# Optimization experiments

Measured on AMD Instinct MI355X. Metric: run time of the kernel, lower is better.

Reference implementation:

```python
import jax, jax.numpy as jnp
import numpy as np

B, T, D, H = 64, 512, 1024, 1024


def setup_inputs() -> dict:
    key = jax.random.key(0)
    ks = jax.random.split(key, 6)
    std = 1.0 / np.sqrt(H)  # torch reset_parameters: uniform(-std, std)
    x = jax.random.normal(ks[0], (B, T, D), dtype=jnp.float32)
    teacher_mask = jax.random.uniform(ks[1], (B, T), dtype=jnp.float32)
    Wx = jax.random.uniform(ks[2], (4 * H, D), minval=-std, maxval=std, dtype=jnp.float32)
    bx = jax.random.uniform(ks[3], (4 * H,), minval=-std, maxval=std, dtype=jnp.float32)
    Wh = jax.random.uniform(ks[4], (4 * H, H), minval=-std, maxval=std, dtype=jnp.float32)
    bh = jax.random.uniform(ks[5], (4 * H,), minval=-std, maxval=std, dtype=jnp.float32)
    return {"x": x, "teacher_mask": teacher_mask, "Wx": Wx, "bx": bx, "Wh": Wh, "bh": bh}


def reference(x, teacher_mask, Wx, bx, Wh, bh):
    b = x.shape[0]
    h0 = jnp.zeros((b, H), dtype=x.dtype)
    c0 = jnp.zeros((b, H), dtype=x.dtype)
    xs = jnp.swapaxes(x, 0, 1)                      # [T, B, D]
    ms = jnp.swapaxes(teacher_mask, 0, 1)[..., None]  # [T, B, 1]

    def step(carry, inp):
        hn, cn = carry
        x_t, m = inp
        # teacher_fn(seq, (hn, cn), x_t) := hn (previous hidden); blend with mask
        new_x = m * hn + (1.0 - m) * x_t
        gates = new_x @ Wx.T + bx + hn @ Wh.T + bh   # [B, 4H]
        i, f, g, o = jnp.split(gates, 4, axis=1)     # torch chunk order: i, f, g, o
        i = jax.nn.sigmoid(i)
        f = jax.nn.sigmoid(f)
        g = jnp.tanh(g)
        o = jax.nn.sigmoid(o)
        cy = cn * f + i * g
        hy = o * jnp.tanh(cy)
        return (hy, cy), hy

    (hn, cn), ys = jax.lax.scan(step, (h0, c0), (xs, ms))
    out = jnp.swapaxes(ys, 0, 1)                     # [B, T, H]
    return out, hn, cn
```

## Files before the change

### kernel.cpp

```cpp
#include <hip/hip_runtime.h>
#include <stdint.h>


#define B_ 64
#define T_ 512
#define D_ 1024
#define H_ 1024
#define NBLK 256
#define UPB 8
#define NROW 32
#define NTHR 512

typedef __attribute__((ext_vector_type(8))) short short8;
typedef __attribute__((ext_vector_type(16))) float f32x16;

#define GBUF_OFF 131072
#define BIAS_OFF 147968
#define SMEM_BYTES 148096

#define WS_ABUF 4096
#define PANEL (64 * 2048)

__device__ __forceinline__ unsigned f2bf(float f) {
  unsigned u = __float_as_uint(f);
  return (u + 0x7FFFu + ((u >> 16) & 1u)) >> 16;
}
__device__ __forceinline__ float sigf(float x) { return 1.0f / (1.0f + __expf(-x)); }
__device__ __forceinline__ float tanhf_(float x) { return 1.0f - 2.0f / (__expf(2.0f * x) + 1.0f); }

__global__ void prep_a0(const float* __restrict__ x, const float* __restrict__ tm,
                        unsigned short* __restrict__ abuf) {
  int i = blockIdx.x * blockDim.x + threadIdx.x;
  if (i >= B_ * D_) return;
  int d = i & (D_ - 1), b = i >> 10;
  float m = tm[b * T_];
  float a = (1.0f - m) * x[(size_t)b * T_ * D_ + d];
  abuf[((d >> 3) * 64 + b) * 8 + (d & 7)] = (unsigned short)f2bf(a);
}

__global__ __launch_bounds__(NTHR, 1)
void lstm_persist(const float* __restrict__ xf,
                  const float* __restrict__ tm,
                  const float* __restrict__ Wx, const float* __restrict__ bxp,
                  const float* __restrict__ Wh, const float* __restrict__ bhp,
                  float* __restrict__ out,
                  unsigned short* __restrict__ abuf,
                  unsigned* __restrict__ flags,
                  unsigned* __restrict__ gen)
{
  extern __shared__ char smem[];
  float* gbuf     = (float*)(smem + GBUF_OFF);
  float* bias_lds = (float*)(smem + BIAS_OFF);

  const int tid = threadIdx.x;
  const int bid = blockIdx.x;
  const int ug  = bid >> 1;
  const int bg  = bid & 1;

  for (int i = 0; i < 64; ++i) {
    const int s  = i * NTHR + tid;
    const int dw = s & 3, n = (s >> 2) & 31, kgs = (s >> 7) & 1;
    const int js = (s >> 8) & 15, kos = s >> 12;
    const int grow = (n >> 3) * H_ + ug * UPB + (n & 7);
    const int k = kos * 256 + js * 16 + kgs * 8 + dw * 2;
    const float* src = (k < D_) ? (Wx + (size_t)grow * D_ + k)
                                : (Wh + (size_t)grow * H_ + (k - D_));
    float2 v = *(const float2*)src;
    *(unsigned*)(smem + (size_t)s * 4) = f2bf(v.x) | (f2bf(v.y) << 16);
  }
  if (tid < NROW) {
    const int grow = (tid >> 3) * H_ + ug * UPB + (tid & 7);
    bias_lds[tid] = bxp[grow] + bhp[grow];
  }

  const int lane = tid & 63;
  const int wid  = tid >> 6;
  const int ko   = wid;
  const int l31  = lane & 31;
  const int kg   = lane >> 5;
  const int b0   = bg * 32;

  const unsigned wbase = (unsigned)(ko * 16384 + kg * 512 + l31 * 16);
#define LDW(J) (*(const short8*)(smem + wbase + (unsigned)((J) * 1024)))
  const size_t aull0 = ((size_t)(ko * 32 + kg) * 64 + (b0 + l31)) * 2;

  const int act = (tid < 256);
  const int cb2 = (tid >> 3) & 31;
  const int cu  = tid & 7;
  const int b   = b0 + cb2;
  const int hu  = ug * UPB + cu;
  float ccell = 0.0f, hv = 0.0f;

  unsigned cur = 0;
  __syncthreads();

  for (int t = 0; t < T_; ++t) {
    const int nxt = (t + 1 < T_) ? (t + 1) : t;
    const unsigned tgt = (unsigned)(t + 1);

    const unsigned long long* ap =
        (const unsigned long long*)(abuf + (size_t)cur * PANEL) + aull0;
    short8 af[16];
#pragma unroll
    for (int j = 0; j < 16; ++j) {
      unsigned long long lo = __hip_atomic_load(ap + (size_t)j * 256,
                                                __ATOMIC_RELAXED, __HIP_MEMORY_SCOPE_AGENT);
      unsigned long long hi = __hip_atomic_load(ap + (size_t)j * 256 + 1,
                                                __ATOMIC_RELAXED, __HIP_MEMORY_SCOPE_AGENT);
      ((unsigned long long*)&af[j])[0] = lo;
      ((unsigned long long*)&af[j])[1] = hi;
    }

    f32x16 acc = {0,0,0,0,0,0,0,0,0,0,0,0,0,0,0,0};
#pragma unroll
    for (int j = 0; j < 16; ++j)
      acc = __builtin_amdgcn_mfma_f32_32x32x16_bf16(af[j], LDW(j), acc, 0, 0, 0);

    float mv = 0.0f, xv = 0.0f;
    if (act) {
      mv = tm[b * T_ + nxt];
      xv = xf[((size_t)b * T_ + nxt) * D_ + hu];
    }

    const int s = wid & 3;
    if (wid < 4) {
#pragma unroll
      for (int e = 0; e < 16; ++e) {
        const int br = (e & 3) + 8 * (e >> 2) + 4 * kg;
        float g = acc[e];
        if (wid == 0) g += bias_lds[l31];
        gbuf[(s * 32 + br) * 33 + l31] = g;
      }
    }
    __syncthreads();
    if (wid >= 4) {
#pragma unroll
      for (int e = 0; e < 16; ++e) {
        const int br = (e & 3) + 8 * (e >> 2) + 4 * kg;
        gbuf[(s * 32 + br) * 33 + l31] += acc[e];
      }
    }
    __syncthreads();

    if (act) {
      float gi = 0.0f, gf = 0.0f, gg = 0.0f, go = 0.0f;
#pragma unroll
      for (int sl = 0; sl < 4; ++sl) {
        const float* row = gbuf + (sl * 32 + cb2) * 33;
        gi += row[cu];      gf += row[8 + cu];
        gg += row[16 + cu]; go += row[24 + cu];
      }
      const float iv = sigf(gi), fv = sigf(gf), gv = tanhf_(gg), ov = sigf(go);
      ccell = ccell * fv + iv * gv;
      hv = ov * tanhf_(ccell);

      const float av = mv * hv + (1.0f - mv) * xv;
      unsigned short* dst = abuf + (size_t)(cur ^ 1u) * PANEL;
      __hip_atomic_store(dst + (((hu >> 3) * 64) + b) * 8 + (hu & 7),
                         (unsigned short)f2bf(av),
                         __ATOMIC_RELAXED, __HIP_MEMORY_SCOPE_AGENT);
      __hip_atomic_store(dst + ((((1024 + hu) >> 3) * 64) + b) * 8 + (hu & 7),
                         (unsigned short)f2bf(hv),
                         __ATOMIC_RELAXED, __HIP_MEMORY_SCOPE_AGENT);
    }

    __syncthreads();

    if (bid == 0) {
      if (wid == 0) {
        for (;;) {
          unsigned v0 = (lane == 0) ? tgt
              : __hip_atomic_load(flags + lane, __ATOMIC_RELAXED, __HIP_MEMORY_SCOPE_AGENT);
          unsigned v1 = __hip_atomic_load(flags + 64 + lane,
                                          __ATOMIC_RELAXED, __HIP_MEMORY_SCOPE_AGENT);
          unsigned v2 = __hip_atomic_load(flags + 128 + lane,
                                          __ATOMIC_RELAXED, __HIP_MEMORY_SCOPE_AGENT);
          unsigned v3 = __hip_atomic_load(flags + 192 + lane,
                                          __ATOMIC_RELAXED, __HIP_MEMORY_SCOPE_AGENT);
          if (__all((v0 >= tgt) && (v1 >= tgt) && (v2 >= tgt) && (v3 >= tgt))) break;
          __builtin_amdgcn_s_sleep(1);
        }
        if (lane == 0)
          __hip_atomic_store(gen, tgt, __ATOMIC_RELAXED, __HIP_MEMORY_SCOPE_AGENT);
      }
      if (act) out[((size_t)b * T_ + t) * H_ + hu] = hv;
    } else {
      if (tid == 0)
        __hip_atomic_store(flags + bid, tgt,
                           __ATOMIC_RELAXED, __HIP_MEMORY_SCOPE_AGENT);
      if (act) out[((size_t)b * T_ + t) * H_ + hu] = hv;
      if (wid == 0) {
        while (__hip_atomic_load(gen, __ATOMIC_RELAXED, __HIP_MEMORY_SCOPE_AGENT) < tgt)
          __builtin_amdgcn_s_sleep(1);
      }
    }
    __syncthreads();
    __builtin_amdgcn_sched_barrier(0);

    cur ^= 1u;
  }

  if (act) {
    out[(size_t)B_ * T_ * H_ + (size_t)b * H_ + hu] = hv;
    out[(size_t)B_ * T_ * H_ + (size_t)B_ * H_ + (size_t)b * H_ + hu] = ccell;
  }
}

extern "C" void kernel_launch(void* const* d_in, const int* in_sizes, int n_in,
                              void* d_out, int out_size, void* d_ws, size_t ws_size,
                              hipStream_t stream) {
  const float* x  = (const float*)d_in[0];
  const float* tm = (const float*)d_in[1];
  const float* Wx = (const float*)d_in[2];
  const float* bx = (const float*)d_in[3];
  const float* Wh = (const float*)d_in[4];
  const float* bh = (const float*)d_in[5];
  float* out = (float*)d_out;
  char* ws = (char*)d_ws;

  unsigned* flags      = (unsigned*)ws;
  unsigned* gen        = (unsigned*)(ws + 2048);
  unsigned short* abuf = (unsigned short*)(ws + WS_ABUF);

  hipMemsetAsync(ws, 0, WS_ABUF + 2 * PANEL * 2, stream);
  prep_a0<<<dim3((B_ * D_ + 255) / 256), dim3(256), 0, stream>>>(x, tm, abuf);
  lstm_persist<<<dim3(NBLK), dim3(NTHR), SMEM_BYTES, stream>>>(
      x, tm, Wx, bx, Wh, bh, out, abuf, flags, gen);
}
```

Baseline: 2.722 ms.

## Split mask blend into separate x and h matmuls, precompute x-projection off critical path

Uses linearity to rewrite (m*h+(1-m)*x)@Wx^T as m*(h@Wx^T)+(1-m)*(x@Wx^T). The x term for the next step is computed with MFMA while blocks wait at the grid barrier, so only the h-dependent K=1024 half (two 8-step MFMA chains) sits on the serial critical path. A pre-pass converts x to a bf16 panel layout when workspace allows, and the mask is transposed and staged in LDS. The h exchange buffer shrinks to just h. In exchange it adds a full-x conversion pass and extra MFMA work per step.

```diff
diff --git a/kernel.cpp b/kernel.cpp
--- a/kernel.cpp
+++ b/kernel.cpp
@@ -14,12 +14,16 @@
 typedef __attribute__((ext_vector_type(8))) short short8;
 typedef __attribute__((ext_vector_type(16))) float f32x16;
 
+#define WH_OFF 65536
 #define GBUF_OFF 131072
-#define BIAS_OFF 147968
-#define SMEM_BYTES 148096
-
-#define WS_ABUF 4096
-#define PANEL (64 * 2048)
+#define MLDS_OFF 147968
+#define BIAS_OFF 148480
+#define SMEM_BYTES 148608
+
+#define WS_MT 4096
+#define WS_HBUF 135168
+#define WS_XP 397312
+#define HSLOT 65536
 
 __device__ __forceinline__ unsigned f2bf(float f) {
   unsigned u = __float_as_uint(f);
@@ -28,28 +32,43 @@
 __device__ __forceinline__ float sigf(float x) { return 1.0f / (1.0f + __expf(-x)); }
 __device__ __forceinline__ float tanhf_(float x) { return 1.0f - 2.0f / (__expf(2.0f * x) + 1.0f); }
 
-__global__ void prep_a0(const float* __restrict__ x, const float* __restrict__ tm,
-                        unsigned short* __restrict__ abuf) {
+__global__ void prep_m(const float* __restrict__ tm, float* __restrict__ mT) {
   int i = blockIdx.x * blockDim.x + threadIdx.x;
-  if (i >= B_ * D_) return;
-  int d = i & (D_ - 1), b = i >> 10;
-  float m = tm[b * T_];
-  float a = (1.0f - m) * x[(size_t)b * T_ * D_ + d];
-  abuf[((d >> 3) * 64 + b) * 8 + (d & 7)] = (unsigned short)f2bf(a);
-}
-
+  if (i >= B_ * T_) return;
+  int b = i >> 9, t = i & (T_ - 1);
+  mT[t * B_ + b] = tm[i];
+}
+
+__global__ void prep_x(const float* __restrict__ x, unsigned short* __restrict__ xp) {
+  int i = blockIdx.x * blockDim.x + threadIdx.x;
+  if (i >= B_ * T_ * D_ / 8) return;
+  const int dblk = i & 127, t = (i >> 7) & (T_ - 1), b = i >> 16;
+  const float* src = x + ((size_t)b * T_ + t) * D_ + dblk * 8;
+  float4 a0 = *(const float4*)src;
+  float4 a1 = *(const float4*)(src + 4);
+  short8 r;
+  r[0] = (short)f2bf(a0.x); r[1] = (short)f2bf(a0.y);
+  r[2] = (short)f2bf(a0.z); r[3] = (short)f2bf(a0.w);
+  r[4] = (short)f2bf(a1.x); r[5] = (short)f2bf(a1.y);
+  r[6] = (short)f2bf(a1.z); r[7] = (short)f2bf(a1.w);
+  *(short8*)(xp + ((size_t)(t * 128 + dblk) * 64 + b) * 8) = r;
+}
+
+template<int XB>
 __global__ __launch_bounds__(NTHR, 1)
 void lstm_persist(const float* __restrict__ xf,
-                  const float* __restrict__ tm,
+                  const unsigned short* __restrict__ xp,
+                  const float* __restrict__ mT,
                   const float* __restrict__ Wx, const float* __restrict__ bxp,
                   const float* __restrict__ Wh, const float* __restrict__ bhp,
                   float* __restrict__ out,
-                  unsigned short* __restrict__ abuf,
+                  unsigned short* __restrict__ hbuf,
                   unsigned* __restrict__ flags,
                   unsigned* __restrict__ gen)
 {
   extern __shared__ char smem[];
   float* gbuf     = (float*)(smem + GBUF_OFF);
+  float* m_lds    = (float*)(smem + MLDS_OFF);
   float* bias_lds = (float*)(smem + BIAS_OFF);
 
   const int tid = threadIdx.x;
@@ -57,16 +76,17 @@
   const int ug  = bid >> 1;
   const int bg  = bid & 1;
 
-  for (int i = 0; i < 64; ++i) {
+  for (int i = 0; i < 32; ++i) {
     const int s  = i * NTHR + tid;
     const int dw = s & 3, n = (s >> 2) & 31, kgs = (s >> 7) & 1;
-    const int js = (s >> 8) & 15, kos = s >> 12;
+    const int js = (s >> 8) & 7, kos = s >> 11;
     const int grow = (n >> 3) * H_ + ug * UPB + (n & 7);
-    const int k = kos * 256 + js * 16 + kgs * 8 + dw * 2;
-    const float* src = (k < D_) ? (Wx + (size_t)grow * D_ + k)
-                                : (Wh + (size_t)grow * H_ + (k - D_));
-    float2 v = *(const float2*)src;
-    *(unsigned*)(smem + (size_t)s * 4) = f2bf(v.x) | (f2bf(v.y) << 16);
+    const int k = kos * 128 + js * 16 + kgs * 8 + dw * 2;
+    const unsigned byte = (unsigned)(kos * 8192 + js * 1024 + kgs * 512 + n * 16 + dw * 4);
+    float2 v = *(const float2*)(Wx + (size_t)grow * D_ + k);
+    *(unsigned*)(smem + byte) = f2bf(v.x) | (f2bf(v.y) << 16);
+    v = *(const float2*)(Wh + (size_t)grow * H_ + k);
+    *(unsigned*)(smem + WH_OFF + byte) = f2bf(v.x) | (f2bf(v.y) << 16);
   }
   if (tid < NROW) {
     const int grow = (tid >> 3) * H_ + ug * UPB + (tid & 7);
@@ -80,9 +100,11 @@
   const int kg   = lane >> 5;
   const int b0   = bg * 32;
 
-  const unsigned wbase = (unsigned)(ko * 16384 + kg * 512 + l31 * 16);
-#define LDW(J) (*(const short8*)(smem + wbase + (unsigned)((J) * 1024)))
-  const size_t aull0 = ((size_t)(ko * 32 + kg) * 64 + (b0 + l31)) * 2;
+  const unsigned wxbase = (unsigned)(ko * 8192 + kg * 512 + l31 * 16);
+#define LWX(J) (*(const short8*)(smem + wxbase + (unsigned)((J) * 1024)))
+#define LWH(J) (*(const short8*)(smem + WH_OFF + wxbase + (unsigned)((J) * 1024)))
+  const size_t hull0 = ((size_t)(ko * 16 + kg) * 64 + (b0 + l31)) * 2;
+  const size_t xsh0 = ((size_t)(ko * 16 + kg) * 64 + (b0 + l31)) * 8;
 
   const int act = (tid < 256);
   const int cb2 = (tid >> 3) & 31;
@@ -91,43 +113,64 @@
   const int hu  = ug * UPB + cu;
   float ccell = 0.0f, hv = 0.0f;
 
-  unsigned cur = 0;
+  __syncthreads();
+
+  f32x16 accX = {0,0,0,0,0,0,0,0,0,0,0,0,0,0,0,0};
+  if (XB) {
+    const unsigned short* xb = xp + xsh0;
+#pragma unroll
+    for (int j = 0; j < 8; ++j)
+      accX = __builtin_amdgcn_mfma_f32_32x32x16_bf16(
+          *(const short8*)(xb + j * 1024), LWX(j), accX, 0, 0, 0);
+  } else {
+    const float* xsrc = xf + (size_t)(b0 + l31) * T_ * D_ + ko * 128 + kg * 8;
+#pragma unroll
+    for (int j = 0; j < 8; ++j) {
+      float4 a0 = *(const float4*)(xsrc + j * 16);
+      float4 a1 = *(const float4*)(xsrc + j * 16 + 4);
+      short8 r;
+      r[0] = (short)f2bf(a0.x); r[1] = (short)f2bf(a0.y);
+      r[2] = (short)f2bf(a0.z); r[3] = (short)f2bf(a0.w);
+      r[4] = (short)f2bf(a1.x); r[5] = (short)f2bf(a1.y);
+      r[6] = (short)f2bf(a1.z); r[7] = (short)f2bf(a1.w);
+      accX = __builtin_amdgcn_mfma_f32_32x32x16_bf16(r, LWX(j), accX, 0, 0, 0);
+    }
+  }
+  if (tid < B_) m_lds[tid] = mT[tid];
   __syncthreads();
 
   for (int t = 0; t < T_; ++t) {
     const int nxt = (t + 1 < T_) ? (t + 1) : t;
     const unsigned tgt = (unsigned)(t + 1);
 
-    const unsigned long long* ap =
-        (const unsigned long long*)(abuf + (size_t)cur * PANEL) + aull0;
-    short8 af[16];
-#pragma unroll
-    for (int j = 0; j < 16; ++j) {
-      unsigned long long lo = __hip_atomic_load(ap + (size_t)j * 256,
+    const unsigned long long* hp =
+        (const unsigned long long*)(hbuf + (size_t)(t & 1) * HSLOT) + hull0;
+    short8 hf[8];
+#pragma unroll
+    for (int j = 0; j < 8; ++j) {
+      unsigned long long lo = __hip_atomic_load(hp + (size_t)j * 256,
                                                 __ATOMIC_RELAXED, __HIP_MEMORY_SCOPE_AGENT);
-      unsigned long long hi = __hip_atomic_load(ap + (size_t)j * 256 + 1,
+      unsigned long long hi = __hip_atomic_load(hp + (size_t)j * 256 + 1,
                                                 __ATOMIC_RELAXED, __HIP_MEMORY_SCOPE_AGENT);
-      ((unsigned long long*)&af[j])[0] = lo;
-      ((unsigned long long*)&af[j])[1] = hi;
-    }
-
-    f32x16 acc = {0,0,0,0,0,0,0,0,0,0,0,0,0,0,0,0};
-#pragma unroll
-    for (int j = 0; j < 16; ++j)
-      acc = __builtin_amdgcn_mfma_f32_32x32x16_bf16(af[j], LDW(j), acc, 0, 0, 0);
-
-    float mv = 0.0f, xv = 0.0f;
-    if (act) {
-      mv = tm[b * T_ + nxt];
-      xv = xf[((size_t)b * T_ + nxt) * D_ + hu];
-    }
-
+      ((unsigned long long*)&hf[j])[0] = lo;
+      ((unsigned long long*)&hf[j])[1] = hi;
+    }
+    f32x16 accA = {0,0,0,0,0,0,0,0,0,0,0,0,0,0,0,0};
+    f32x16 accC = {0,0,0,0,0,0,0,0,0,0,0,0,0,0,0,0};
+#pragma unroll
+    for (int j = 0; j < 8; ++j) {
+      accA = __builtin_amdgcn_mfma_f32_32x32x16_bf16(hf[j], LWX(j), accA, 0, 0, 0);
+      accC = __builtin_amdgcn_mfma_f32_32x32x16_bf16(hf[j], LWH(j), accC, 0, 0, 0);
+    }
+
+    const float* ml = m_lds + (t & 1) * B_;
     const int s = wid & 3;
     if (wid < 4) {
 #pragma unroll
       for (int e = 0; e < 16; ++e) {
         const int br = (e & 3) + 8 * (e >> 2) + 4 * kg;
-        float g = acc[e];
+        const float mv = ml[b0 + br];
+        float g = mv * accA[e] + (1.0f - mv) * accX[e] + accC[e];
         if (wid == 0) g += bias_lds[l31];
         gbuf[(s * 32 + br) * 33 + l31] = g;
       }
@@ -137,7 +180,8 @@
 #pragma unroll
       for (int e = 0; e < 16; ++e) {
         const int br = (e & 3) + 8 * (e >> 2) + 4 * kg;
-        gbuf[(s * 32 + br) * 33 + l31] += acc[e];
+        const float mv = ml[b0 + br];
+        gbuf[(s * 32 + br) * 33 + l31] += mv * accA[e] + (1.0f - mv) * accX[e] + accC[e];
       }
     }
     __syncthreads();
@@ -153,13 +197,8 @@
       const float iv = sigf(gi), fv = sigf(gf), gv = tanhf_(gg), ov = sigf(go);
       ccell = ccell * fv + iv * gv;
       hv = ov * tanhf_(ccell);
-
-      const float av = mv * hv + (1.0f - mv) * xv;
-      unsigned short* dst = abuf + (size_t)(cur ^ 1u) * PANEL;
-      __hip_atomic_store(dst + (((hu >> 3) * 64) + b) * 8 + (hu & 7),
-                         (unsigned short)f2bf(av),
-                         __ATOMIC_RELAXED, __HIP_MEMORY_SCOPE_AGENT);
-      __hip_atomic_store(dst + ((((1024 + hu) >> 3) * 64) + b) * 8 + (hu & 7),
+      __hip_atomic_store(hbuf + (size_t)((t + 1) & 1) * HSLOT +
+                             ((hu >> 3) * 64 + b) * 8 + (hu & 7),
                          (unsigned short)f2bf(hv),
                          __ATOMIC_RELAXED, __HIP_MEMORY_SCOPE_AGENT);
     }
@@ -183,21 +222,44 @@
         if (lane == 0)
           __hip_atomic_store(gen, tgt, __ATOMIC_RELAXED, __HIP_MEMORY_SCOPE_AGENT);
       }
-      if (act) out[((size_t)b * T_ + t) * H_ + hu] = hv;
     } else {
       if (tid == 0)
         __hip_atomic_store(flags + bid, tgt,
                            __ATOMIC_RELAXED, __HIP_MEMORY_SCOPE_AGENT);
-      if (act) out[((size_t)b * T_ + t) * H_ + hu] = hv;
-      if (wid == 0) {
-        while (__hip_atomic_load(gen, __ATOMIC_RELAXED, __HIP_MEMORY_SCOPE_AGENT) < tgt)
-          __builtin_amdgcn_s_sleep(1);
-      }
+    }
+
+    if (act) out[((size_t)b * T_ + t) * H_ + hu] = hv;
+    f32x16 accXn = {0,0,0,0,0,0,0,0,0,0,0,0,0,0,0,0};
+    if (XB) {
+      const unsigned short* xb = xp + (size_t)nxt * (128 * 64 * 8) + xsh0;
+#pragma unroll
+      for (int j = 0; j < 8; ++j)
+        accXn = __builtin_amdgcn_mfma_f32_32x32x16_bf16(
+            *(const short8*)(xb + j * 1024), LWX(j), accXn, 0, 0, 0);
+    } else {
+      const float* xsrc = xf + ((size_t)(b0 + l31) * T_ + nxt) * D_ + ko * 128 + kg * 8;
+#pragma unroll
+      for (int j = 0; j < 8; ++j) {
+        float4 a0 = *(const float4*)(xsrc + j * 16);
+        float4 a1 = *(const float4*)(xsrc + j * 16 + 4);
+        short8 r;
+        r[0] = (short)f2bf(a0.x); r[1] = (short)f2bf(a0.y);
+        r[2] = (short)f2bf(a0.z); r[3] = (short)f2bf(a0.w);
+        r[4] = (short)f2bf(a1.x); r[5] = (short)f2bf(a1.y);
+        r[6] = (short)f2bf(a1.z); r[7] = (short)f2bf(a1.w);
+        accXn = __builtin_amdgcn_mfma_f32_32x32x16_bf16(r, LWX(j), accXn, 0, 0, 0);
+      }
+    }
+    if (tid < B_) m_lds[((t + 1) & 1) * B_ + tid] = mT[nxt * B_ + tid];
+
+    if (bid != 0 && wid == 0) {
+      while (__hip_atomic_load(gen, __ATOMIC_RELAXED, __HIP_MEMORY_SCOPE_AGENT) < tgt)
+        __builtin_amdgcn_s_sleep(1);
     }
     __syncthreads();
     __builtin_amdgcn_sched_barrier(0);
 
-    cur ^= 1u;
+    accX = accXn;
   }
 
   if (act) {
@@ -220,10 +282,22 @@
 
   unsigned* flags      = (unsigned*)ws;
   unsigned* gen        = (unsigned*)(ws + 2048);
-  unsigned short* abuf = (unsigned short*)(ws + WS_ABUF);
-
-  hipMemsetAsync(ws, 0, WS_ABUF + 2 * PANEL * 2, stream);
-  prep_a0<<<dim3((B_ * D_ + 255) / 256), dim3(256), 0, stream>>>(x, tm, abuf);
-  lstm_persist<<<dim3(NBLK), dim3(NTHR), SMEM_BYTES, stream>>>(
-      x, tm, Wx, bx, Wh, bh, out, abuf, flags, gen);
-}
+  float* mT            = (float*)(ws + WS_MT);
+  unsigned short* hbuf = (unsigned short*)(ws + WS_HBUF);
+  unsigned short* xp   = (unsigned short*)(ws + WS_XP);
+
+  const size_t need_xp = (size_t)WS_XP + 2ull * B_ * T_ * D_;
+  const bool use_xp = ws_size >= need_xp;
+
+  hipMemsetAsync(ws, 0, WS_HBUF + 2 * HSLOT * 2, stream);
+  prep_m<<<dim3((B_ * T_ + 255) / 256), dim3(256), 0, stream>>>(tm, mT);
+  if (use_xp) {
+    const int n = B_ * T_ * D_ / 8;
+    prep_x<<<dim3((n + 255) / 256), dim3(256), 0, stream>>>(x, xp);
+    lstm_persist<1><<<dim3(NBLK), dim3(NTHR), SMEM_BYTES, stream>>>(
+        x, xp, mT, Wx, bx, Wh, bh, out, hbuf, flags, gen);
+  } else {
+    lstm_persist<0><<<dim3(NBLK), dim3(NTHR), SMEM_BYTES, stream>>>(
+        x, xp, mT, Wx, bx, Wh, bh, out, hbuf, flags, gen);
+  }
+}
```

New measurement: 2.827 ms. 1.04x slower.
